# Performance work log

Hardware: AMD Instinct MI355X
Metric: run time of the kernel (lower is better)

## Reference

```python
import jax, jax.numpy as jnp
import numpy as np

B = 32768
STATE_DIM = 64
ACTION_DIM = 16
HIDDEN = 512
ENSEMBLE = 7
TOP_K = 5
IN_DIM = STATE_DIM + ACTION_DIM          # 80
OUT_DIM = 2 * (STATE_DIM + 1)            # 130 (mu | log_std)


def setup_inputs() -> dict:
    key = jax.random.key(0)
    ks = jax.random.split(key, 12)
    state = jax.random.normal(ks[0], (B, STATE_DIM), dtype=jnp.float32)
    action = jax.random.normal(ks[1], (B, ACTION_DIM), dtype=jnp.float32)
    eps = jax.random.normal(ks[2], (B, STATE_DIM + 1), dtype=jnp.float32)
    # per-sample random expert among the selected subset [0, TOP_K)
    idx = jax.random.randint(ks[3], (B,), 0, TOP_K).astype(jnp.int64)
    # stacked expert params (kaiming-ish scale = 1/sqrt(fan_in))
    W1 = jax.random.normal(ks[4], (ENSEMBLE, IN_DIM, HIDDEN), dtype=jnp.float32) / np.sqrt(IN_DIM)
    b1 = jnp.zeros((ENSEMBLE, HIDDEN), dtype=jnp.float32)
    W2 = jax.random.normal(ks[5], (ENSEMBLE, HIDDEN, HIDDEN), dtype=jnp.float32) / np.sqrt(HIDDEN)
    b2 = jnp.zeros((ENSEMBLE, HIDDEN), dtype=jnp.float32)
    W3 = jax.random.normal(ks[6], (ENSEMBLE, HIDDEN, OUT_DIM), dtype=jnp.float32) / np.sqrt(HIDDEN)
    b3 = jnp.zeros((ENSEMBLE, OUT_DIM), dtype=jnp.float32)
    return {"state": state, "action": action, "eps": eps,
            "W1": W1, "b1": b1, "W2": W2, "b2": b2, "W3": W3, "b3": b3,
            "idx": idx}


def reference(state, action, eps, W1, b1, W2, b2, W3, b3, idx):
    # DynamicsEnsemble.predict: per-sample random expert, Gaussian sample.
    x = jnp.concatenate([state, action], axis=-1)            # [B, IN_DIM]
    # run all experts densely, then gather the routed expert per sample
    h = jax.nn.relu(jnp.einsum('bi,eih->beh', x, W1) + b1)   # [B, E, H]
    h = jax.nn.relu(jnp.einsum('beh,ehk->bek', h, W2) + b2)  # [B, E, H]
    o = jnp.einsum('bek,eko->beo', h, W3) + b3               # [B, E, OUT]
    out = jnp.take_along_axis(o, idx[:, None, None].astype(jnp.int32), axis=1)[:, 0]  # [B, OUT]
    d = state.shape[-1] + 1
    mu = out[:, :d]
    log_std = jnp.clip(out[:, d:], -20.0, 2.0)
    y = mu + jnp.exp(log_std) * eps                          # sampled [delta_state, reward]
    next_state = state + y[:, : state.shape[-1]]
    reward = y[:, state.shape[-1]:]                          # [B, 1]
    return next_state, reward
```

## Files before the change

### kernel.cpp

```cpp
#include <hip/hip_runtime.h>
#include <math.h>

#define B_ROWS     32768
#define STATE_DIM  64
#define ACTION_DIM 16
#define HIDDEN     512
#define ENSEMBLE   7
#define TOP_K      5
#define IN_DIM     80
#define OUT_DIM    130
#define D_OUT      65

#define BM         32
#define MTHREADS   512
#define NTILES     (B_ROWS / BM + TOP_K)

#define L1_K8 12
#define L2_K8 64
#define L3_K8 64
#define L3_N  144

#define N_W1 (TOP_K * L1_K8 * HIDDEN * 8)
#define N_W2 (TOP_K * L2_K8 * HIDDEN * 8)
#define N_W3 (TOP_K * L3_K8 * L3_N * 8)

#define OFF_CNT    0
#define OFF_BUCKET 256
#define OFF_W1     (OFF_BUCKET + ENSEMBLE * B_ROWS * 4)
#define OFF_W2     (OFF_W1 + N_W1 * 2)
#define OFF_W3     (OFF_W2 + N_W2 * 2)
#define WS_NEEDED  ((size_t)(OFF_W3 + N_W3 * 2))

#define BUCKET_BLOCKS ((B_ROWS + 255) / 256)
#define PACK_G        (TOP_K * (L1_K8*HIDDEN + L2_K8*HIDDEN + L3_K8*L3_N))
#define PACK_BLOCKS   ((PACK_G + 255) / 256)

typedef __attribute__((ext_vector_type(8))) _Float16 half8;
typedef __attribute__((ext_vector_type(4))) float f32x4;

__global__ void prep_kernel(const int* __restrict__ idx,
                            int* __restrict__ cnt,
                            int* __restrict__ bucket,
                            const float* __restrict__ W1, const float* __restrict__ W2,
                            const float* __restrict__ W3,
                            _Float16* __restrict__ w1, _Float16* __restrict__ w2,
                            _Float16* __restrict__ w3) {
    if (blockIdx.x < BUCKET_BLOCKS) {
        int b = blockIdx.x * 256 + threadIdx.x;
        int lane = threadIdx.x & 63;
        int e = -1;
        if (b < B_ROWS) e = min(max(idx[b], 0), TOP_K - 1);
        #pragma unroll
        for (int ev = 0; ev < TOP_K; ++ev) {
            unsigned long long m = __ballot(e == ev);
            if (m == 0ull) continue;
            int leader = __ffsll((unsigned long long)m) - 1;
            int base = 0;
            if (lane == leader) base = atomicAdd(&cnt[ev], __popcll(m));
            base = __shfl(base, leader);
            if (e == ev) {
                int rank = __popcll(m & ((1ull << lane) - 1ull));
                bucket[ev * B_ROWS + base + rank] = b;
            }
        }
        return;
    }
    const int G1 = L1_K8 * HIDDEN;
    const int G2 = L2_K8 * HIDDEN;
    const int G3 = L3_K8 * L3_N;
    const int GPE = G1 + G2 + G3;
    int g = (blockIdx.x - BUCKET_BLOCKS) * 256 + threadIdx.x;
    if (g >= TOP_K * GPE) return;
    int e = g / GPE, r = g % GPE;

    const float* src; _Float16* dd;
    size_t dst; int k8, n, Kreal, Nreal, srcN;
    if (r < G1) {
        k8 = r / HIDDEN; n = r % HIDDEN;
        src = W1 + (size_t)e * IN_DIM * HIDDEN; Kreal = IN_DIM; Nreal = HIDDEN; srcN = HIDDEN;
        dd = w1; dst = (((size_t)e * L1_K8 + k8) * HIDDEN + n) * 8;
    } else if (r < G1 + G2) {
        int rr = r - G1; k8 = rr / HIDDEN; n = rr % HIDDEN;
        src = W2 + (size_t)e * HIDDEN * HIDDEN; Kreal = HIDDEN; Nreal = HIDDEN; srcN = HIDDEN;
        dd = w2; dst = (((size_t)e * L2_K8 + k8) * HIDDEN + n) * 8;
    } else {
        int rr = r - G1 - G2; k8 = rr / L3_N; n = rr % L3_N;
        src = W3 + (size_t)e * HIDDEN * OUT_DIM; Kreal = HIDDEN; Nreal = OUT_DIM; srcN = OUT_DIM;
        dd = w3; dst = (((size_t)e * L3_K8 + k8) * L3_N + n) * 8;
    }
    half8 hv;
    #pragma unroll
    for (int j = 0; j < 8; ++j) {
        int k = k8 * 8 + j;
        float v = (k < Kreal && n < Nreal) ? src[(size_t)k * srcN + n] : 0.f;
        hv[j] = (_Float16)v;
    }
    *(half8*)(dd + dst) = hv;
}

template<int ASTR, bool SWZ, int KSTEPS>
__device__ __forceinline__ void gemm_compute(
    const char* A,
    const _Float16* __restrict__ B, int Bn, const float* __restrict__ bias,
    f32x4 (&acc)[2][4], int lane, int col0)
{
    const int lc = lane & 15, kg = lane >> 4;
    #pragma unroll
    for (int ctl = 0; ctl < 4; ++ctl) {
        float b = bias[col0 + ctl * 16 + lc];
        acc[0][ctl] = (f32x4){b, b, b, b};
        acc[1][ctl] = acc[0][ctl];
    }
    const size_t bstep = (size_t)4 * Bn * 8;
    const _Float16* bp = B + ((size_t)kg * Bn + col0 + lc) * 8;

    half8 buf[2][4];
    #pragma unroll
    for (int ctl = 0; ctl < 4; ++ctl) buf[0][ctl] = *(const half8*)(bp + ctl * 128);

    #pragma unroll
    for (int ks = 0; ks < KSTEPS; ++ks) {
        const int cur = ks & 1, nxt = cur ^ 1;
        if (ks + 1 < KSTEPS) {
            const _Float16* pn = bp + (size_t)(ks + 1) * bstep;
            #pragma unroll
            for (int ctl = 0; ctl < 4; ++ctl) buf[nxt][ctl] = *(const half8*)(pn + ctl * 128);
        }
        half8 ah[2];
        #pragma unroll
        for (int rt = 0; rt < 2; ++rt) {
            int row = rt * 16 + lc;
            int lin = row * ASTR + ks * 64 + kg * 16;
            if (SWZ) lin ^= (row & 7) << 4;
            ah[rt] = *(const half8*)(A + lin);
        }
        #pragma unroll
        for (int rt = 0; rt < 2; ++rt)
        #pragma unroll
        for (int ctl = 0; ctl < 4; ++ctl)
            acc[rt][ctl] = __builtin_amdgcn_mfma_f32_16x16x32_f16(ah[rt], buf[cur][ctl], acc[rt][ctl], 0, 0, 0);
    }
}

__device__ __forceinline__ void store_h(char* O, f32x4 (&acc)[2][4], int lane, int col0) {
    const int lc = lane & 15, kg = lane >> 4;
    #pragma unroll
    for (int rt = 0; rt < 2; ++rt)
    #pragma unroll
    for (int ctl = 0; ctl < 4; ++ctl)
    #pragma unroll
    for (int q = 0; q < 4; ++q) {
        int row = rt * 16 + kg * 4 + q;
        int col = col0 + ctl * 16 + lc;
        float v = fmaxf(acc[rt][ctl][q], 0.f);
        int lin = (row * 1024 + col * 2) ^ ((row & 7) << 4);
        *(_Float16*)(O + lin) = (_Float16)v;
    }
}

__device__ __forceinline__ int xcd_swz(int orig) {
    const int nx = 8, q = NTILES / nx, r = NTILES % nx;
    int xcd = orig % nx, pos = orig / nx;
    int base = (xcd < r) ? xcd * (q + 1) : r * (q + 1) + (xcd - r) * q;
    return base + pos;
}

__launch_bounds__(MTHREADS, 2)
__global__ void mlp_mfma_kernel(const float* __restrict__ state,
                                const float* __restrict__ action,
                                const float* __restrict__ eps,
                                const float* __restrict__ b1,
                                const float* __restrict__ b2,
                                const float* __restrict__ b3,
                                const _Float16* __restrict__ w1,
                                const _Float16* __restrict__ w2,
                                const _Float16* __restrict__ w3,
                                const int* __restrict__ cnt, const int* __restrict__ bucket,
                                float* __restrict__ out) {
    __shared__ char smem[39936];
    char* xs = smem;
    char* hs = smem + 7168;
    float* os = (float*)(smem + 7168);

    const int j = xcd_swz(blockIdx.x);
    int e = TOP_K, base = 0;
    {
        int acct = 0;
        #pragma unroll
        for (int ev = 0; ev < TOP_K; ++ev) {
            int tiles = (cnt[ev] + BM - 1) / BM;
            if (e == TOP_K && j < acct + tiles) { e = ev; base = acct; }
            acct += tiles;
        }
    }
    if (e >= TOP_K) return;
    const int n    = cnt[e];
    const int tile = j - base;
    const int m0   = tile * BM;
    if (m0 >= n) return;
    const int nrows = min(BM, n - m0);
    const int t = threadIdx.x;
    const int lane = t & 63;
    const int wv = t >> 6;
    const int col0 = wv * 64;
    const int* brow = bucket + (size_t)e * B_ROWS;

    for (int i = t; i < BM * 112; i += MTHREADS) {
        int r = i / 112, c = i % 112;
        int rb = brow[min(m0 + r, n - 1)];
        float v = 0.f;
        if (c < STATE_DIM)      v = state[(size_t)rb * STATE_DIM + c];
        else if (c < IN_DIM)    v = action[(size_t)rb * ACTION_DIM + (c - STATE_DIM)];
        *(_Float16*)(xs + r * 224 + c * 2) = (_Float16)v;
    }
    __syncthreads();

    f32x4 acc[2][4];

    gemm_compute<224, false, 3>(xs,
        w1 + (size_t)e * L1_K8 * HIDDEN * 8,
        HIDDEN, b1 + (size_t)e * HIDDEN, acc, lane, col0);
    store_h(hs, acc, lane, col0);
    __syncthreads();

    gemm_compute<1024, true, 16>(hs,
        w2 + (size_t)e * L2_K8 * HIDDEN * 8,
        HIDDEN, b2 + (size_t)e * HIDDEN, acc, lane, col0);
    __syncthreads();
    store_h(hs, acc, lane, col0);
    __syncthreads();

    {
        const _Float16* Bw = w3 + (size_t)e * L3_K8 * L3_N * 8;
        const float* b3e = b3 + (size_t)e * OUT_DIM;
        const int lc = lane & 15, kg = lane >> 4;
        const int rt  = wv & 1;
        const int ct0 = wv >> 1;
        const bool third = (wv < 2);
        f32x4 o0 = {0.f,0.f,0.f,0.f}, o1 = o0, o2 = o0;
        const size_t bstep = (size_t)4 * L3_N * 8;
        const _Float16* bp0 = Bw + ((size_t)kg * L3_N + ct0 * 16 + lc) * 8;
        const _Float16* bp1 = Bw + ((size_t)kg * L3_N + (ct0 + 4) * 16 + lc) * 8;
        const _Float16* bp2 = Bw + ((size_t)kg * L3_N + 8 * 16 + lc) * 8;

        half8 p0[2], p1[2], p2[2];
        p0[0] = *(const half8*)(bp0);
        p1[0] = *(const half8*)(bp1);
        if (third) p2[0] = *(const half8*)(bp2);

        #pragma unroll
        for (int ks = 0; ks < 16; ++ks) {
            const int cur = ks & 1, nxt = cur ^ 1;
            if (ks + 1 < 16) {
                p0[nxt] = *(const half8*)(bp0 + (size_t)(ks + 1) * bstep);
                p1[nxt] = *(const half8*)(bp1 + (size_t)(ks + 1) * bstep);
                if (third) p2[nxt] = *(const half8*)(bp2 + (size_t)(ks + 1) * bstep);
            }
            int row = rt * 16 + lc;
            int lin = (row * 1024 + ks * 64 + kg * 16) ^ ((row & 7) << 4);
            half8 ah = *(const half8*)(hs + lin);
            o0 = __builtin_amdgcn_mfma_f32_16x16x32_f16(ah, p0[cur], o0, 0, 0, 0);
            o1 = __builtin_amdgcn_mfma_f32_16x16x32_f16(ah, p1[cur], o1, 0, 0, 0);
            if (third) o2 = __builtin_amdgcn_mfma_f32_16x16x32_f16(ah, p2[cur], o2, 0, 0, 0);
        }
        __syncthreads();
        {
            int col = ct0 * 16 + lc;
            #pragma unroll
            for (int q = 0; q < 4; ++q) {
                int row = rt * 16 + kg * 4 + q;
                os[row * 132 + col] = o0[q] + b3e[col];
                if (col + 64 < OUT_DIM) os[row * 132 + col + 64] = o1[q] + b3e[col + 64];
            }
            if (third) {
                int col2 = 128 + lc;
                if (col2 < OUT_DIM) {
                    #pragma unroll
                    for (int q = 0; q < 4; ++q) {
                        int row = rt * 16 + kg * 4 + q;
                        os[row * 132 + col2] = o2[q] + b3e[col2];
                    }
                }
            }
        }
    }
    __syncthreads();

    for (int i = t; i < BM * D_OUT; i += MTHREADS) {
        int r = i / D_OUT, c = i % D_OUT;
        if (r >= nrows) continue;
        int rb = brow[m0 + r];
        float mu = os[r * 132 + c];
        float ls = fminf(fmaxf(os[r * 132 + c + D_OUT], -20.f), 2.f);
        float y  = fmaf(expf(ls), eps[(size_t)rb * D_OUT + c], mu);
        if (c < STATE_DIM) {
            out[(size_t)rb * STATE_DIM + c] = state[(size_t)rb * STATE_DIM + c] + y;
        } else {
            out[(size_t)B_ROWS * STATE_DIM + rb] = y;
        }
    }
}

#define FB_BM      16
#define FB_THREADS 256
#define FB_TILES   ((B_ROWS + FB_BM - 1) / FB_BM)

__launch_bounds__(FB_THREADS, 2)
__global__ void mlp_fp32_kernel(const float* __restrict__ state,
                                const float* __restrict__ action,
                                const float* __restrict__ eps,
                                const float* __restrict__ W1, const float* __restrict__ b1,
                                const float* __restrict__ W2, const float* __restrict__ b2,
                                const float* __restrict__ W3, const float* __restrict__ b3,
                                const int* __restrict__ cnt, const int* __restrict__ bucket,
                                float* __restrict__ out) {
    __shared__ float xs[FB_BM][IN_DIM];
    __shared__ float h1[FB_BM][HIDDEN];
    __shared__ float h2[FB_BM][HIDDEN];
    __shared__ float os[FB_BM][OUT_DIM];
    __shared__ int   rows[FB_BM];

    const int e    = blockIdx.x / FB_TILES;
    const int tile = blockIdx.x % FB_TILES;
    const int n    = cnt[e];
    const int m0   = tile * FB_BM;
    if (m0 >= n) return;
    const int nrows = min(FB_BM, n - m0);
    const int t = threadIdx.x;

    if (t < FB_BM) rows[t] = (t < nrows) ? bucket[e * B_ROWS + m0 + t] : bucket[e * B_ROWS + m0];
    __syncthreads();

    for (int i = t; i < FB_BM * IN_DIM; i += FB_THREADS) {
        int r = i / IN_DIM, c = i % IN_DIM;
        int rb = rows[r];
        xs[r][c] = (c < STATE_DIM) ? state[(size_t)rb * STATE_DIM + c]
                                   : action[(size_t)rb * ACTION_DIM + (c - STATE_DIM)];
    }
    __syncthreads();

    const int c0 = 2 * t;
    {
        const float* We = W1 + (size_t)e * IN_DIM * HIDDEN;
        float acc0[FB_BM], acc1[FB_BM];
        const float bias0 = b1[(size_t)e * HIDDEN + c0];
        const float bias1 = b1[(size_t)e * HIDDEN + c0 + 1];
        #pragma unroll
        for (int r = 0; r < FB_BM; ++r) { acc0[r] = bias0; acc1[r] = bias1; }
        for (int k = 0; k < IN_DIM; k += 4) {
            float2 w0 = *(const float2*)&We[(size_t)(k + 0) * HIDDEN + c0];
            float2 w1v = *(const float2*)&We[(size_t)(k + 1) * HIDDEN + c0];
            float2 w2v = *(const float2*)&We[(size_t)(k + 2) * HIDDEN + c0];
            float2 w3v = *(const float2*)&We[(size_t)(k + 3) * HIDDEN + c0];
            #pragma unroll
            for (int r = 0; r < FB_BM; ++r) {
                float4 x = *(const float4*)&xs[r][k];
                acc0[r] = fmaf(x.x, w0.x, acc0[r]); acc1[r] = fmaf(x.x, w0.y, acc1[r]);
                acc0[r] = fmaf(x.y, w1v.x, acc0[r]); acc1[r] = fmaf(x.y, w1v.y, acc1[r]);
                acc0[r] = fmaf(x.z, w2v.x, acc0[r]); acc1[r] = fmaf(x.z, w2v.y, acc1[r]);
                acc0[r] = fmaf(x.w, w3v.x, acc0[r]); acc1[r] = fmaf(x.w, w3v.y, acc1[r]);
            }
        }
        #pragma unroll
        for (int r = 0; r < FB_BM; ++r)
            *(float2*)&h1[r][c0] = make_float2(fmaxf(acc0[r], 0.f), fmaxf(acc1[r], 0.f));
    }
    __syncthreads();
    {
        const float* We = W2 + (size_t)e * HIDDEN * HIDDEN;
        float acc0[FB_BM], acc1[FB_BM];
        const float bias0 = b2[(size_t)e * HIDDEN + c0];
        const float bias1 = b2[(size_t)e * HIDDEN + c0 + 1];
        #pragma unroll
        for (int r = 0; r < FB_BM; ++r) { acc0[r] = bias0; acc1[r] = bias1; }
        for (int k = 0; k < HIDDEN; k += 4) {
            float2 w0 = *(const float2*)&We[(size_t)(k + 0) * HIDDEN + c0];
            float2 w1v = *(const float2*)&We[(size_t)(k + 1) * HIDDEN + c0];
            float2 w2v = *(const float2*)&We[(size_t)(k + 2) * HIDDEN + c0];
            float2 w3v = *(const float2*)&We[(size_t)(k + 3) * HIDDEN + c0];
            #pragma unroll
            for (int r = 0; r < FB_BM; ++r) {
                float4 x = *(const float4*)&h1[r][k];
                acc0[r] = fmaf(x.x, w0.x, acc0[r]); acc1[r] = fmaf(x.x, w0.y, acc1[r]);
                acc0[r] = fmaf(x.y, w1v.x, acc0[r]); acc1[r] = fmaf(x.y, w1v.y, acc1[r]);
                acc0[r] = fmaf(x.z, w2v.x, acc0[r]); acc1[r] = fmaf(x.z, w2v.y, acc1[r]);
                acc0[r] = fmaf(x.w, w3v.x, acc0[r]); acc1[r] = fmaf(x.w, w3v.y, acc1[r]);
            }
        }
        #pragma unroll
        for (int r = 0; r < FB_BM; ++r)
            *(float2*)&h2[r][c0] = make_float2(fmaxf(acc0[r], 0.f), fmaxf(acc1[r], 0.f));
    }
    __syncthreads();
    {
        const float* We = W3 + (size_t)e * HIDDEN * OUT_DIM;
        for (int i = t; i < FB_BM * OUT_DIM; i += FB_THREADS) {
            int r = i / OUT_DIM, c = i % OUT_DIM;
            float acc = b3[(size_t)e * OUT_DIM + c];
            for (int k = 0; k < HIDDEN; k += 4) {
                float4 h = *(const float4*)&h2[r][k];
                acc = fmaf(h.x, We[(size_t)(k + 0) * OUT_DIM + c], acc);
                acc = fmaf(h.y, We[(size_t)(k + 1) * OUT_DIM + c], acc);
                acc = fmaf(h.z, We[(size_t)(k + 2) * OUT_DIM + c], acc);
                acc = fmaf(h.w, We[(size_t)(k + 3) * OUT_DIM + c], acc);
            }
            os[r][c] = acc;
        }
    }
    __syncthreads();
    for (int i = t; i < FB_BM * D_OUT; i += FB_THREADS) {
        int r = i / D_OUT, c = i % D_OUT;
        if (r >= nrows) continue;
        int rb = rows[r];
        float mu = os[r][c];
        float ls = fminf(fmaxf(os[r][c + D_OUT], -20.f), 2.f);
        float y  = fmaf(expf(ls), eps[(size_t)rb * D_OUT + c], mu);
        if (c < STATE_DIM) out[(size_t)rb * STATE_DIM + c] = state[(size_t)rb * STATE_DIM + c] + y;
        else               out[(size_t)B_ROWS * STATE_DIM + rb] = y;
    }
}

extern "C" void kernel_launch(void* const* d_in, const int* in_sizes, int n_in,
                              void* d_out, int out_size, void* d_ws, size_t ws_size,
                              hipStream_t stream) {
    const float* state  = (const float*)d_in[0];
    const float* action = (const float*)d_in[1];
    const float* eps    = (const float*)d_in[2];
    const float* W1     = (const float*)d_in[3];
    const float* b1     = (const float*)d_in[4];
    const float* W2     = (const float*)d_in[5];
    const float* b2     = (const float*)d_in[6];
    const float* W3     = (const float*)d_in[7];
    const float* b3     = (const float*)d_in[8];
    const int*   idx    = (const int*)d_in[9];
    float* out = (float*)d_out;

    int* cnt    = (int*)((char*)d_ws + OFF_CNT);
    int* bucket = (int*)((char*)d_ws + OFF_BUCKET);

    hipMemsetAsync(cnt, 0, ENSEMBLE * sizeof(int), stream);

    if (ws_size >= WS_NEEDED) {
        _Float16* w1 = (_Float16*)((char*)d_ws + OFF_W1);
        _Float16* w2 = (_Float16*)((char*)d_ws + OFF_W2);
        _Float16* w3 = (_Float16*)((char*)d_ws + OFF_W3);

        prep_kernel<<<BUCKET_BLOCKS + PACK_BLOCKS, 256, 0, stream>>>(
            idx, cnt, bucket, W1, W2, W3, w1, w2, w3);

        mlp_mfma_kernel<<<NTILES, MTHREADS, 0, stream>>>(
            state, action, eps, b1, b2, b3, w1, w2, w3, cnt, bucket, out);
    } else {
        prep_kernel<<<BUCKET_BLOCKS, 256, 0, stream>>>(
            idx, cnt, bucket, W1, W2, W3, (_Float16*)0, (_Float16*)0, (_Float16*)0);
        mlp_fp32_kernel<<<TOP_K * FB_TILES, FB_THREADS, 0, stream>>>(
            state, action, eps, W1, b1, W2, b2, W3, b3, cnt, bucket, out);
    }
}
```

Before: 114.3 us.

## Enlarge row tile to 128 with 16 waves for more weight reuse

Measured after the change: 191.3 us. +67.4%, slower.

```diff
diff --git a/kernel.cpp b/kernel.cpp
--- a/kernel.cpp
+++ b/kernel.cpp
@@ -11,8 +11,8 @@
 #define OUT_DIM    130
 #define D_OUT      65
 
-#define BM         32
-#define MTHREADS   512
+#define BM         128
+#define MTHREADS   1024
 #define NTILES     (B_ROWS / BM + TOP_K)
 
 #define L1_K8 12
@@ -102,11 +102,11 @@
 __device__ __forceinline__ void gemm_compute(
     const char* A,
     const _Float16* __restrict__ B, int Bn, const float* __restrict__ bias,
-    f32x4 (&acc)[2][4], int lane, int col0)
+    f32x4 (&acc)[2][8], int lane, int row0, int col0)
 {
     const int lc = lane & 15, kg = lane >> 4;
     #pragma unroll
-    for (int ctl = 0; ctl < 4; ++ctl) {
+    for (int ctl = 0; ctl < 8; ++ctl) {
         float b = bias[col0 + ctl * 16 + lc];
         acc[0][ctl] = (f32x4){b, b, b, b};
         acc[1][ctl] = acc[0][ctl];
@@ -114,22 +114,16 @@
     const size_t bstep = (size_t)4 * Bn * 8;
     const _Float16* bp = B + ((size_t)kg * Bn + col0 + lc) * 8;
 
-    half8 buf[2][4];
-    #pragma unroll
-    for (int ctl = 0; ctl < 4; ++ctl) buf[0][ctl] = *(const half8*)(bp + ctl * 128);
-
     #pragma unroll
     for (int ks = 0; ks < KSTEPS; ++ks) {
-        const int cur = ks & 1, nxt = cur ^ 1;
-        if (ks + 1 < KSTEPS) {
-            const _Float16* pn = bp + (size_t)(ks + 1) * bstep;
-            #pragma unroll
-            for (int ctl = 0; ctl < 4; ++ctl) buf[nxt][ctl] = *(const half8*)(pn + ctl * 128);
-        }
+        half8 bc[8];
+        #pragma unroll
+        for (int ctl = 0; ctl < 8; ++ctl)
+            bc[ctl] = *(const half8*)(bp + (size_t)ks * bstep + ctl * 128);
         half8 ah[2];
         #pragma unroll
         for (int rt = 0; rt < 2; ++rt) {
-            int row = rt * 16 + lc;
+            int row = row0 + rt * 16 + lc;
             int lin = row * ASTR + ks * 64 + kg * 16;
             if (SWZ) lin ^= (row & 7) << 4;
             ah[rt] = *(const half8*)(A + lin);
@@ -137,20 +131,20 @@
         #pragma unroll
         for (int rt = 0; rt < 2; ++rt)
         #pragma unroll
-        for (int ctl = 0; ctl < 4; ++ctl)
-            acc[rt][ctl] = __builtin_amdgcn_mfma_f32_16x16x32_f16(ah[rt], buf[cur][ctl], acc[rt][ctl], 0, 0, 0);
-    }
-}
-
-__device__ __forceinline__ void store_h(char* O, f32x4 (&acc)[2][4], int lane, int col0) {
+        for (int ctl = 0; ctl < 8; ++ctl)
+            acc[rt][ctl] = __builtin_amdgcn_mfma_f32_16x16x32_f16(ah[rt], bc[ctl], acc[rt][ctl], 0, 0, 0);
+    }
+}
+
+__device__ __forceinline__ void store_h(char* O, f32x4 (&acc)[2][8], int lane, int row0, int col0) {
     const int lc = lane & 15, kg = lane >> 4;
     #pragma unroll
     for (int rt = 0; rt < 2; ++rt)
     #pragma unroll
-    for (int ctl = 0; ctl < 4; ++ctl)
+    for (int ctl = 0; ctl < 8; ++ctl)
     #pragma unroll
     for (int q = 0; q < 4; ++q) {
-        int row = rt * 16 + kg * 4 + q;
+        int row = row0 + rt * 16 + kg * 4 + q;
         int col = col0 + ctl * 16 + lc;
         float v = fmaxf(acc[rt][ctl][q], 0.f);
         int lin = (row * 1024 + col * 2) ^ ((row & 7) << 4);
@@ -165,7 +159,7 @@
     return base + pos;
 }
 
-__launch_bounds__(MTHREADS, 2)
+__launch_bounds__(MTHREADS)
 __global__ void mlp_mfma_kernel(const float* __restrict__ state,
                                 const float* __restrict__ action,
                                 const float* __restrict__ eps,
@@ -177,10 +171,10 @@
                                 const _Float16* __restrict__ w3,
                                 const int* __restrict__ cnt, const int* __restrict__ bucket,
                                 float* __restrict__ out) {
-    __shared__ char smem[39936];
+    __shared__ char smem[159744];
     char* xs = smem;
-    char* hs = smem + 7168;
-    float* os = (float*)(smem + 7168);
+    char* hs = smem + 28672;
+    float* os = (float*)(smem + 28672);
 
     const int j = xcd_swz(blockIdx.x);
     int e = TOP_K, base = 0;
@@ -202,7 +196,8 @@
     const int t = threadIdx.x;
     const int lane = t & 63;
     const int wv = t >> 6;
-    const int col0 = wv * 64;
+    const int row0 = (wv >> 2) * 32;
+    const int col0 = (wv & 3) * 128;
     const int* brow = bucket + (size_t)e * B_ROWS;
 
     for (int i = t; i < BM * 112; i += MTHREADS) {
@@ -215,71 +210,71 @@
     }
     __syncthreads();
 
-    f32x4 acc[2][4];
+    f32x4 acc[2][8];
 
     gemm_compute<224, false, 3>(xs,
         w1 + (size_t)e * L1_K8 * HIDDEN * 8,
-        HIDDEN, b1 + (size_t)e * HIDDEN, acc, lane, col0);
-    store_h(hs, acc, lane, col0);
+        HIDDEN, b1 + (size_t)e * HIDDEN, acc, lane, row0, col0);
+    store_h(hs, acc, lane, row0, col0);
     __syncthreads();
 
     gemm_compute<1024, true, 16>(hs,
         w2 + (size_t)e * L2_K8 * HIDDEN * 8,
-        HIDDEN, b2 + (size_t)e * HIDDEN, acc, lane, col0);
-    __syncthreads();
-    store_h(hs, acc, lane, col0);
+        HIDDEN, b2 + (size_t)e * HIDDEN, acc, lane, row0, col0);
+    __syncthreads();
+    store_h(hs, acc, lane, row0, col0);
     __syncthreads();
 
     {
         const _Float16* Bw = w3 + (size_t)e * L3_K8 * L3_N * 8;
         const float* b3e = b3 + (size_t)e * OUT_DIM;
         const int lc = lane & 15, kg = lane >> 4;
-        const int rt  = wv & 1;
-        const int ct0 = wv >> 1;
-        const bool third = (wv < 2);
-        f32x4 o0 = {0.f,0.f,0.f,0.f}, o1 = o0, o2 = o0;
+        const int rtu = wv & 7;
+        const int ct0 = wv >> 3;
+        const bool fifth = (wv < 8);
+        f32x4 o0 = {0.f,0.f,0.f,0.f}, o1 = o0, o2 = o0, o3 = o0, o4 = o0;
         const size_t bstep = (size_t)4 * L3_N * 8;
-        const _Float16* bp0 = Bw + ((size_t)kg * L3_N + ct0 * 16 + lc) * 8;
-        const _Float16* bp1 = Bw + ((size_t)kg * L3_N + (ct0 + 4) * 16 + lc) * 8;
-        const _Float16* bp2 = Bw + ((size_t)kg * L3_N + 8 * 16 + lc) * 8;
-
-        half8 p0[2], p1[2], p2[2];
-        p0[0] = *(const half8*)(bp0);
-        p1[0] = *(const half8*)(bp1);
-        if (third) p2[0] = *(const half8*)(bp2);
+        const _Float16* bp0 = Bw + ((size_t)kg * L3_N + (ct0 + 0) * 16 + lc) * 8;
+        const _Float16* bp1 = Bw + ((size_t)kg * L3_N + (ct0 + 2) * 16 + lc) * 8;
+        const _Float16* bp2 = Bw + ((size_t)kg * L3_N + (ct0 + 4) * 16 + lc) * 8;
+        const _Float16* bp3 = Bw + ((size_t)kg * L3_N + (ct0 + 6) * 16 + lc) * 8;
+        const _Float16* bp4 = Bw + ((size_t)kg * L3_N + 8 * 16 + lc) * 8;
 
         #pragma unroll
         for (int ks = 0; ks < 16; ++ks) {
-            const int cur = ks & 1, nxt = cur ^ 1;
-            if (ks + 1 < 16) {
-                p0[nxt] = *(const half8*)(bp0 + (size_t)(ks + 1) * bstep);
-                p1[nxt] = *(const half8*)(bp1 + (size_t)(ks + 1) * bstep);
-                if (third) p2[nxt] = *(const half8*)(bp2 + (size_t)(ks + 1) * bstep);
-            }
-            int row = rt * 16 + lc;
+            int row = rtu * 16 + lc;
             int lin = (row * 1024 + ks * 64 + kg * 16) ^ ((row & 7) << 4);
             half8 ah = *(const half8*)(hs + lin);
-            o0 = __builtin_amdgcn_mfma_f32_16x16x32_f16(ah, p0[cur], o0, 0, 0, 0);
-            o1 = __builtin_amdgcn_mfma_f32_16x16x32_f16(ah, p1[cur], o1, 0, 0, 0);
-            if (third) o2 = __builtin_amdgcn_mfma_f32_16x16x32_f16(ah, p2[cur], o2, 0, 0, 0);
+            half8 v0 = *(const half8*)(bp0 + (size_t)ks * bstep);
+            half8 v1 = *(const half8*)(bp1 + (size_t)ks * bstep);
+            half8 v2 = *(const half8*)(bp2 + (size_t)ks * bstep);
+            half8 v3 = *(const half8*)(bp3 + (size_t)ks * bstep);
+            o0 = __builtin_amdgcn_mfma_f32_16x16x32_f16(ah, v0, o0, 0, 0, 0);
+            o1 = __builtin_amdgcn_mfma_f32_16x16x32_f16(ah, v1, o1, 0, 0, 0);
+            o2 = __builtin_amdgcn_mfma_f32_16x16x32_f16(ah, v2, o2, 0, 0, 0);
+            o3 = __builtin_amdgcn_mfma_f32_16x16x32_f16(ah, v3, o3, 0, 0, 0);
+            if (fifth) {
+                half8 v4 = *(const half8*)(bp4 + (size_t)ks * bstep);
+                o4 = __builtin_amdgcn_mfma_f32_16x16x32_f16(ah, v4, o4, 0, 0, 0);
+            }
         }
         __syncthreads();
         {
-            int col = ct0 * 16 + lc;
+            const int rowb = rtu * 16 + kg * 4;
             #pragma unroll
             for (int q = 0; q < 4; ++q) {
-                int row = rt * 16 + kg * 4 + q;
-                os[row * 132 + col] = o0[q] + b3e[col];
-                if (col + 64 < OUT_DIM) os[row * 132 + col + 64] = o1[q] + b3e[col + 64];
-            }
-            if (third) {
-                int col2 = 128 + lc;
-                if (col2 < OUT_DIM) {
-                    #pragma unroll
-                    for (int q = 0; q < 4; ++q) {
-                        int row = rt * 16 + kg * 4 + q;
-                        os[row * 132 + col2] = o2[q] + b3e[col2];
-                    }
+                int row = rowb + q;
+                int c0 = (ct0 + 0) * 16 + lc;
+                int c1 = (ct0 + 2) * 16 + lc;
+                int c2 = (ct0 + 4) * 16 + lc;
+                int c3 = (ct0 + 6) * 16 + lc;
+                os[row * 132 + c0] = o0[q] + b3e[c0];
+                os[row * 132 + c1] = o1[q] + b3e[c1];
+                os[row * 132 + c2] = o2[q] + b3e[c2];
+                if (c3 < OUT_DIM) os[row * 132 + c3] = o3[q] + b3e[c3];
+                if (fifth) {
+                    int c4 = 128 + lc;
+                    if (c4 < OUT_DIM) os[row * 132 + c4] = o4[q] + b3e[c4];
                 }
             }
         }
```
